# Performance work log

Measured on AMD Instinct MI355X. Metric: run time of the kernel, lower is better.

Reference implementation:

```python
import jax, jax.numpy as jnp
import numpy as np

THETA0 = 3.0
THETA = 5.0


def _boundaries(targets, num_classes):
    # targets: (B,H,W) int -> boundary magnitude (B,H,W) float32
    B, H, W = targets.shape
    oh = jax.nn.one_hot(targets, num_classes, dtype=jnp.float32)  # (B,H,W,C)
    x = oh.transpose(0, 3, 1, 2).reshape(B * num_classes, 1, H, W)
    # replicate padding == F.pad(..., mode='replicate')
    xp = jnp.pad(x, ((0, 0), (0, 0), (1, 1), (1, 1)), mode='edge')
    sobel_x = jnp.array([[-1, 0, 1], [-2, 0, 2], [-1, 0, 1]], jnp.float32)
    sobel_y = jnp.array([[-1, -2, -1], [0, 0, 0], [1, 2, 1]], jnp.float32)
    kern = jnp.stack([sobel_x, sobel_y])[:, None]  # (2,1,3,3) OIHW
    g = jax.lax.conv_general_dilated(
        xp, kern, window_strides=(1, 1), padding='VALID',
        dimension_numbers=('NCHW', 'OIHW', 'NCHW'))  # (B*C,2,H,W)
    grad_mag = jnp.sqrt(g[:, 0] ** 2 + g[:, 1] ** 2).reshape(B, num_classes, H, W)
    # running per-class max == max over class axis
    return grad_mag.max(axis=1)


def setup_inputs() -> dict:
    key = jax.random.key(0)
    k1, k2 = jax.random.split(key)
    logits = jax.random.normal(k1, (8, 20, 512, 512), dtype=jnp.float32)
    targets = jax.random.randint(k2, (8, 512, 512), 0, 20)
    return {"logits": logits, "targets": targets}


def reference(logits, targets):
    num_classes = logits.shape[1]
    boundaries = _boundaries(targets, num_classes)          # (B,H,W)
    weight_map = jnp.exp(jnp.clip(boundaries * THETA0, 0.0, THETA))
    log_probs = jax.nn.log_softmax(logits, axis=1)          # (B,C,H,W)
    # nll_loss with reduction='none': -log_probs gathered at target class
    nll = -jnp.take_along_axis(log_probs, targets[:, None, :, :], axis=1)[:, 0]
    weighted = nll * weight_map
    return weighted.mean()
```

## Files before the change

### kernel.cpp

```cpp
#include <hip/hip_runtime.h>
#include <math.h>

namespace {
constexpr int B = 8, C = 20, H = 512, W = 512;
constexpr int HW = H * W;
constexpr int GROUPS = B * H * W / 4;
constexpr int NBLK = GROUPS / 256;
constexpr float INV_N = 1.0f / (float)(B * H * W);

typedef float f32x4 __attribute__((ext_vector_type(4)));

__device__ constexpr float SX[9] = {-1, 0, 1, -2, 0, 2, -1, 0, 1};
__device__ constexpr float SY[9] = {-1, -2, -1, 0, 0, 0, 1, 2, 1};

constexpr float W0 = 1.0f;
constexpr float W1 = 20.085536923187668f;
constexpr float W2 = 69.591390994170540f;
constexpr float W3 = 148.41315910257660f;
}

__global__ void bl_zero_kernel(float* out) {
    if (threadIdx.x == 0) out[0] = 0.0f;
}

template <bool ATOMIC>
__global__ __launch_bounds__(256) void bl_main(const float* __restrict__ logits,
                                               const int* __restrict__ targets,
                                               float* __restrict__ outp) {
    const int g = blockIdx.x * 256 + threadIdx.x;
    const int w4 = (g & (W / 4 - 1)) * 4;
    const int hh = (g >> 7) & (H - 1);
    const int b  = g >> 16;

    int tr[3][6];
    const int tbase = b * H * W;
    #pragma unroll
    for (int i = 0; i < 3; ++i) {
        int hy = hh + i - 1;
        hy = hy < 0 ? 0 : (hy >= H ? H - 1 : hy);
        const int* rp = targets + tbase + hy * W;
        #pragma unroll
        for (int j = 0; j < 6; ++j) {
            int wx = w4 + j - 1;
            wx = wx < 0 ? 0 : (wx >= W ? W - 1 : wx);
            tr[i][j] = rp[wx];
        }
    }

    float wgt[4];
    int tc[4];
    #pragma unroll
    for (int p = 0; p < 4; ++p) {
        tc[p] = tr[1][p + 1];
        float best = 0.0f;
        #pragma unroll
        for (int k = 0; k < 9; ++k) {
            const int cc = tr[k / 3][p + k % 3];
            float gx = 0.0f, gy = 0.0f;
            #pragma unroll
            for (int q = 0; q < 9; ++q) {
                if (q == 4) continue;
                const float mt = (tr[q / 3][p + q % 3] == cc) ? 1.0f : 0.0f;
                gx = fmaf(mt, SX[q], gx);
                gy = fmaf(mt, SY[q], gy);
            }
            best = fmaxf(best, fmaf(gx, gx, gy * gy));
        }
        wgt[p] = best > 2.5f ? W3 : (best > 1.5f ? W2 : (best > 0.5f ? W1 : W0));
    }

    float s[4]  = {0.0f, 0.0f, 0.0f, 0.0f};
    float lt[4] = {0.0f, 0.0f, 0.0f, 0.0f};
    const float* lp = logits + (size_t)b * C * HW + (size_t)hh * W + w4;

    #pragma unroll 1
    for (int half = 0; half < 2; ++half) {
        f32x4 v[10];
        const float* hp = lp + (size_t)half * 10 * HW;
        #pragma unroll
        for (int i = 0; i < 10; ++i)
            v[i] = __builtin_nontemporal_load(
                reinterpret_cast<const f32x4*>(hp + (size_t)i * HW));
        const int cbase = half * 10;
        #pragma unroll
        for (int i = 0; i < 10; ++i) {
            s[0] += __expf(v[i].x);
            s[1] += __expf(v[i].y);
            s[2] += __expf(v[i].z);
            s[3] += __expf(v[i].w);
            const int c = cbase + i;
            lt[0] = (c == tc[0]) ? v[i].x : lt[0];
            lt[1] = (c == tc[1]) ? v[i].y : lt[1];
            lt[2] = (c == tc[2]) ? v[i].z : lt[2];
            lt[3] = (c == tc[3]) ? v[i].w : lt[3];
        }
    }

    float acc = 0.0f;
    #pragma unroll
    for (int p = 0; p < 4; ++p)
        acc = fmaf(__logf(s[p]) - lt[p], wgt[p], acc);

    #pragma unroll
    for (int off = 32; off > 0; off >>= 1) acc += __shfl_down(acc, off, 64);
    __shared__ float red[4];
    const int lane = threadIdx.x & 63;
    const int wv = threadIdx.x >> 6;
    if (lane == 0) red[wv] = acc;
    __syncthreads();
    if (threadIdx.x == 0) {
        const float tot = red[0] + red[1] + red[2] + red[3];
        if (ATOMIC) atomicAdd(outp, tot * INV_N);
        else        outp[blockIdx.x] = tot;
    }
}

__global__ __launch_bounds__(256) void bl_reduce(const float* __restrict__ partials,
                                                 float* __restrict__ out) {
    float a = 0.0f;
    #pragma unroll
    for (int i = 0; i < NBLK / 256; ++i)
        a += partials[i * 256 + threadIdx.x];
    #pragma unroll
    for (int off = 32; off > 0; off >>= 1) a += __shfl_down(a, off, 64);
    __shared__ float red[4];
    const int lane = threadIdx.x & 63;
    const int wv = threadIdx.x >> 6;
    if (lane == 0) red[wv] = a;
    __syncthreads();
    if (threadIdx.x == 0)
        out[0] = (red[0] + red[1] + red[2] + red[3]) * INV_N;
}

extern "C" void kernel_launch(void* const* d_in, const int* in_sizes, int n_in,
                              void* d_out, int out_size, void* d_ws, size_t ws_size,
                              hipStream_t stream) {
    const float* logits = (const float*)d_in[0];
    const int* targets = (const int*)d_in[1];
    float* out = (float*)d_out;

    if (ws_size >= (size_t)NBLK * sizeof(float)) {
        float* partials = (float*)d_ws;
        bl_main<false><<<NBLK, 256, 0, stream>>>(logits, targets, partials);
        bl_reduce<<<1, 256, 0, stream>>>(partials, out);
    } else {
        bl_zero_kernel<<<1, 64, 0, stream>>>(out);
        bl_main<true><<<NBLK, 256, 0, stream>>>(logits, targets, out);
    }
}
```

Before: 36.69 us.

## Issue logits loads before Sobel boundary compute and vectorize target loads

Moves the first half of the logits loads ahead of the boundary-weight computation so their memory latency overlaps with the Sobel arithmetic. The second half is issued after the boundary work instead of inside a serial loop. Target rows are now read as one int4 plus two clamped scalars rather than six clamped scalar loads. The Sobel inner loop is written out by hand and skips the center cell. Holding all 20 float4 values live raises register pressure, which may lower occupancy.

New measurement: 33.61 us (median of 2 runs). 8.4% less time.

```diff
diff --git a/kernel.cpp b/kernel.cpp
--- a/kernel.cpp
+++ b/kernel.cpp
@@ -9,9 +9,6 @@
 constexpr float INV_N = 1.0f / (float)(B * H * W);
 
 typedef float f32x4 __attribute__((ext_vector_type(4)));
-
-__device__ constexpr float SX[9] = {-1, 0, 1, -2, 0, 2, -1, 0, 1};
-__device__ constexpr float SY[9] = {-1, -2, -1, 0, 0, 0, 1, 2, 1};
 
 constexpr float W0 = 1.0f;
 constexpr float W1 = 20.085536923187668f;
@@ -32,20 +29,27 @@
     const int hh = (g >> 7) & (H - 1);
     const int b  = g >> 16;
 
+    const int* tb = targets + b * H * W;
+    const int wl = w4 - 1 < 0 ? 0 : w4 - 1;
+    const int wr = w4 + 4 > W - 1 ? W - 1 : w4 + 4;
     int tr[3][6];
-    const int tbase = b * H * W;
     #pragma unroll
     for (int i = 0; i < 3; ++i) {
         int hy = hh + i - 1;
         hy = hy < 0 ? 0 : (hy >= H ? H - 1 : hy);
-        const int* rp = targets + tbase + hy * W;
-        #pragma unroll
-        for (int j = 0; j < 6; ++j) {
-            int wx = w4 + j - 1;
-            wx = wx < 0 ? 0 : (wx >= W ? W - 1 : wx);
-            tr[i][j] = rp[wx];
-        }
+        const int* rp = tb + hy * W;
+        const int4 mid = *reinterpret_cast<const int4*>(rp + w4);
+        tr[i][0] = rp[wl];
+        tr[i][1] = mid.x; tr[i][2] = mid.y; tr[i][3] = mid.z; tr[i][4] = mid.w;
+        tr[i][5] = rp[wr];
     }
+
+    const float* lp = logits + (size_t)b * C * HW + (size_t)hh * W + w4;
+    f32x4 v0[10];
+    #pragma unroll
+    for (int i = 0; i < 10; ++i)
+        v0[i] = __builtin_nontemporal_load(
+            reinterpret_cast<const f32x4*>(lp + (size_t)i * HW));
 
     float wgt[4];
     int tc[4];
@@ -55,45 +59,53 @@
         float best = 0.0f;
         #pragma unroll
         for (int k = 0; k < 9; ++k) {
+            if (k == 4) continue;
             const int cc = tr[k / 3][p + k % 3];
-            float gx = 0.0f, gy = 0.0f;
-            #pragma unroll
-            for (int q = 0; q < 9; ++q) {
-                if (q == 4) continue;
-                const float mt = (tr[q / 3][p + q % 3] == cc) ? 1.0f : 0.0f;
-                gx = fmaf(mt, SX[q], gx);
-                gy = fmaf(mt, SY[q], gy);
-            }
+            const float e0 = (tr[0][p + 0] == cc) ? 1.0f : 0.0f;
+            const float e1 = (tr[0][p + 1] == cc) ? 1.0f : 0.0f;
+            const float e2 = (tr[0][p + 2] == cc) ? 1.0f : 0.0f;
+            const float e3 = (tr[1][p + 0] == cc) ? 1.0f : 0.0f;
+            const float e5 = (tr[1][p + 2] == cc) ? 1.0f : 0.0f;
+            const float e6 = (tr[2][p + 0] == cc) ? 1.0f : 0.0f;
+            const float e7 = (tr[2][p + 1] == cc) ? 1.0f : 0.0f;
+            const float e8 = (tr[2][p + 2] == cc) ? 1.0f : 0.0f;
+            const float gx = (fmaf(2.0f, e5, e2) + e8) - (fmaf(2.0f, e3, e0) + e6);
+            const float gy = (fmaf(2.0f, e7, e6) + e8) - (fmaf(2.0f, e1, e0) + e2);
             best = fmaxf(best, fmaf(gx, gx, gy * gy));
         }
         wgt[p] = best > 2.5f ? W3 : (best > 1.5f ? W2 : (best > 0.5f ? W1 : W0));
     }
 
+    f32x4 v1[10];
+    #pragma unroll
+    for (int i = 0; i < 10; ++i)
+        v1[i] = __builtin_nontemporal_load(
+            reinterpret_cast<const f32x4*>(lp + (size_t)(10 + i) * HW));
+
     float s[4]  = {0.0f, 0.0f, 0.0f, 0.0f};
     float lt[4] = {0.0f, 0.0f, 0.0f, 0.0f};
-    const float* lp = logits + (size_t)b * C * HW + (size_t)hh * W + w4;
-
-    #pragma unroll 1
-    for (int half = 0; half < 2; ++half) {
-        f32x4 v[10];
-        const float* hp = lp + (size_t)half * 10 * HW;
-        #pragma unroll
-        for (int i = 0; i < 10; ++i)
-            v[i] = __builtin_nontemporal_load(
-                reinterpret_cast<const f32x4*>(hp + (size_t)i * HW));
-        const int cbase = half * 10;
-        #pragma unroll
-        for (int i = 0; i < 10; ++i) {
-            s[0] += __expf(v[i].x);
-            s[1] += __expf(v[i].y);
-            s[2] += __expf(v[i].z);
-            s[3] += __expf(v[i].w);
-            const int c = cbase + i;
-            lt[0] = (c == tc[0]) ? v[i].x : lt[0];
-            lt[1] = (c == tc[1]) ? v[i].y : lt[1];
-            lt[2] = (c == tc[2]) ? v[i].z : lt[2];
-            lt[3] = (c == tc[3]) ? v[i].w : lt[3];
-        }
+    #pragma unroll
+    for (int i = 0; i < 10; ++i) {
+        s[0] += __expf(v0[i].x);
+        s[1] += __expf(v0[i].y);
+        s[2] += __expf(v0[i].z);
+        s[3] += __expf(v0[i].w);
+        lt[0] = (i == tc[0]) ? v0[i].x : lt[0];
+        lt[1] = (i == tc[1]) ? v0[i].y : lt[1];
+        lt[2] = (i == tc[2]) ? v0[i].z : lt[2];
+        lt[3] = (i == tc[3]) ? v0[i].w : lt[3];
+    }
+    #pragma unroll
+    for (int i = 0; i < 10; ++i) {
+        const int c = 10 + i;
+        s[0] += __expf(v1[i].x);
+        s[1] += __expf(v1[i].y);
+        s[2] += __expf(v1[i].z);
+        s[3] += __expf(v1[i].w);
+        lt[0] = (c == tc[0]) ? v1[i].x : lt[0];
+        lt[1] = (c == tc[1]) ? v1[i].y : lt[1];
+        lt[2] = (c == tc[2]) ? v1[i].z : lt[2];
+        lt[3] = (c == tc[3]) ? v1[i].w : lt[3];
     }
 
     float acc = 0.0f;
```
